# Performance work log

Hardware: AMD Instinct MI355X
Metric: run time of the kernel (lower is better)

## Reference

```python
import jax, jax.numpy as jnp
import numpy as np

# Fixed feature layout standing in for config.group_tensor_index
IDX_LINE, IDX_LX, IDX_LY, IDX_RX, IDX_RY = 0, 1, 2, 3, 4

B, D, ROUND_DIVIDE = 4_000_000, 16, 8


def setup_inputs() -> dict:
    key = jax.random.key(0)
    k1, k2 = jax.random.split(key)
    z_1 = jax.random.normal(k1, (B, D), dtype=jnp.float32)
    dir = jax.random.uniform(k2, (B, ROUND_DIVIDE), dtype=jnp.float32)
    return {"z_1": z_1, "dir": dir}


def reference(z_1, dir):
    round_divide = dir.shape[1]                 # static
    area_angle = int(180 / round_divide)        # e.g. 22 for 8 zones (matches torch int())
    area_angle_half = area_angle * 0.5

    # direction vector c_2 - c_1 with y flipped (screen coords)
    dx = z_1[:, IDX_RX] - z_1[:, IDX_LX]
    dy = -(z_1[:, IDX_RY] - z_1[:, IDX_LY])

    # cart2pol angle in degrees, mapped to [0, 360)
    phi = jnp.degrees(jnp.arctan2(dy, dx))
    phi = jnp.where(phi < 0, 360.0 + phi, phi)  # == 360 - |phi| for phi<0

    # clockwise shift; .long() truncation == floor since phi >= 0
    phi_clock_shift = (90 + phi.astype(jnp.int32)) % 360

    zone = ((phi_clock_shift.astype(z_1.dtype) + area_angle_half) // area_angle) % round_divide
    zone_id = zone.astype(jnp.int32)            # [B]

    # (dir * one_hot(zone_id)).sum(1) == gather dir at zone_id
    picked = jnp.take_along_axis(dir, zone_id[:, None], axis=1)[:, 0]

    # rows with no line get zero probability
    has_line = z_1[:, IDX_LINE] != 0
    return jnp.where(has_line, picked, jnp.zeros((), dtype=dir.dtype))
```

## Files before the change

### kernel.cpp

```cpp
#include <hip/hip_runtime.h>
#include <math.h>


__global__ __launch_bounds__(256) void slope_zone_kernel(
    const float* __restrict__ z1,
    const float* __restrict__ dir,
    float* __restrict__ out,
    int n)
{
#pragma clang fp contract(off)
    int i = blockIdx.x * blockDim.x + threadIdx.x;
    if (i >= n) return;

    const float4* zrow = reinterpret_cast<const float4*>(z1 + (size_t)i * 16);
    float4 a = zrow[0];
    float ry = z1[(size_t)i * 16 + 4];

    float dx = a.w - a.y;
    float dy = -(ry - a.z);

    float phi_rad = (float)atan2((double)dy, (double)dx);
    float phi = phi_rad * 57.29577951308232f;
    if (phi < 0.0f) phi = 360.0f + phi;

    int t = (int)phi;
    int pcs = (90 + t) % 360;
    int z = (int)(((float)pcs + 11.0f) / 22.0f);
    int zone = z & 7;

    float picked = dir[(size_t)i * 8 + zone];
    out[i] = (a.x != 0.0f) ? picked : 0.0f;
}

extern "C" void kernel_launch(void* const* d_in, const int* in_sizes, int n_in,
                              void* d_out, int out_size, void* d_ws, size_t ws_size,
                              hipStream_t stream) {
    const float* z1  = (const float*)d_in[0];
    const float* dir = (const float*)d_in[1];
    float* out = (float*)d_out;
    int n = out_size;
    int threads = 256;
    int blocks = (n + threads - 1) / threads;
    hipLaunchKernelGGL(slope_zone_kernel, dim3(blocks), dim3(threads), 0, stream,
                       z1, dir, out, n);
}
```

Before: 412.5 us.

## Use float atan2 with double fallback near zone boundaries, vector-load dir row

Computes the angle with single-precision atan2f and only falls back to the double-precision atan2 when a small epsilon window around the angle straddles a zone boundary. This is meant to avoid the costly FP64 transcendental on most rows. It also replaces the modulo and float division with integer arithmetic, and loads the full 8-float dir row as two float4 vectors, picking the element with selects instead of a dependent gather. The exactness of the result depends on the epsilon bounding the atan2f error, and loading the whole dir row reads more bytes than a single-element gather.

```diff
diff --git a/kernel.cpp b/kernel.cpp
--- a/kernel.cpp
+++ b/kernel.cpp
@@ -1,6 +1,12 @@
 #include <hip/hip_runtime.h>
 #include <math.h>
 
+
+__device__ __forceinline__ int zone_of(int t) {
+    int pcs = 90 + t;
+    if (pcs >= 360) pcs -= 360;
+    return ((pcs + 11) / 22) & 7;
+}
 
 __global__ __launch_bounds__(256) void slope_zone_kernel(
     const float* __restrict__ z1,
@@ -16,20 +22,37 @@
     float4 a = zrow[0];
     float ry = z1[(size_t)i * 16 + 4];
 
+    const float4* drow = reinterpret_cast<const float4*>(dir + (size_t)i * 8);
+    float4 d0 = drow[0];
+    float4 d1 = drow[1];
+
     float dx = a.w - a.y;
     float dy = -(ry - a.z);
 
-    float phi_rad = (float)atan2((double)dy, (double)dx);
-    float phi = phi_rad * 57.29577951308232f;
-    if (phi < 0.0f) phi = 360.0f + phi;
+    float pf = atan2f(dy, dx) * 57.29577951308232f;
+    if (pf < 0.0f) pf = 360.0f + pf;
 
-    int t = (int)phi;
-    int pcs = (90 + t) % 360;
-    int z = (int)(((float)pcs + 11.0f) / 22.0f);
-    int zone = z & 7;
+    const float EPS = 0.0078125f;
+    int t_lo = (int)floorf(pf - EPS);
+    int t_hi = (int)floorf(pf + EPS);
+    if (t_lo < 0) t_lo += 360;
+    int zone = zone_of(t_lo);
+    if (zone != zone_of(t_hi)) {
+        float phi_rad = (float)atan2((double)dy, (double)dx);
+        float phi = phi_rad * 57.29577951308232f;
+        if (phi < 0.0f) phi = 360.0f + phi;
+        zone = zone_of((int)phi);
+    }
 
-    float picked = dir[(size_t)i * 8 + zone];
-    out[i] = (a.x != 0.0f) ? picked : 0.0f;
+    float e0 = (zone & 1) ? d0.y : d0.x;
+    float e1 = (zone & 1) ? d0.w : d0.z;
+    float e2 = (zone & 1) ? d1.y : d1.x;
+    float e3 = (zone & 1) ? d1.w : d1.z;
+    float f0 = (zone & 2) ? e1 : e0;
+    float f1 = (zone & 2) ? e3 : e2;
+    float g  = (zone & 4) ? f1 : f0;
+
+    out[i] = (a.x != 0.0f) ? g : 0.0f;
 }
 
 extern "C" void kernel_launch(void* const* d_in, const int* in_sizes, int n_in,
```

New measurement: 412.9 us. About the same (+0.1%).
